# Kernel tuning notes

Hardware: AMD Instinct MI355X
Metric: run time of the kernel (lower is better)

## Reference

```python
import jax, jax.numpy as jnp
import numpy as np

B, T, D, H = 2, 2048, 1024, 16
HD = D // H  # 64
SCALE = 1.0 / np.sqrt(D).astype(np.float32)  # module uses 1/sqrt(mod_dim), not head_dim


def setup_inputs() -> dict:
    key = jax.random.key(0)
    k1, k2, k3 = jax.random.split(key, 3)
    x = jax.random.normal(k1, (B, T, D), dtype=jnp.float32)
    W_attn = jax.random.normal(k2, (3 * D, D), dtype=jnp.float32) * 0.02
    W_out = jax.random.normal(k3, (D, D), dtype=jnp.float32) * 0.02
    return {"x": x, "W_attn": W_attn, "W_out": W_out}


def reference(x, W_attn, W_out):
    b, t, d = x.shape
    # qkv projection (Linear, no bias): x @ W^T
    qkv = jnp.einsum('btd,ed->bte', x, W_attn)  # [b, t, 3d]
    q, k, v = jnp.split(qkv, 3, axis=-1)
    # [b, h, t, hd]
    q = q.reshape(b, t, H, HD).transpose(0, 2, 1, 3)
    k = k.reshape(b, t, H, HD).transpose(0, 2, 1, 3)
    v = v.reshape(b, t, H, HD).transpose(0, 2, 1, 3)
    # raw scores, causal mask applied before scaling (scale*-inf == -inf, so
    # equivalent to the original mask-then-scale order)
    att = jnp.einsum('bhqd,bhkd->bhqk', q, k)
    causal = jnp.tril(jnp.ones((t, t), dtype=bool))
    att = jnp.where(causal[None, None], att * SCALE, -jnp.inf)
    att = jax.nn.softmax(att, axis=-1)
    z = jnp.einsum('bhqk,bhkd->bhqd', att, v)
    z = z.transpose(0, 2, 1, 3).reshape(b, t, d)
    return jnp.einsum('btd,od->bto', z, W_out)
```

## Files before the change

kernel.cpp:

```cpp
#include <hip/hip_runtime.h>
#include <cstddef>

typedef unsigned short u16;
typedef __attribute__((ext_vector_type(4))) float floatx4;
typedef __attribute__((ext_vector_type(8))) short short8;

#define TT 2048
#define DD 1024
#define NH 16
#define ATT_SCALE (1.0f / 32.0f)
#define PSTR 72

__device__ __forceinline__ u16 f2bf(float f) {
  unsigned u = __builtin_bit_cast(unsigned, f);
  u += 0x7fffu + ((u >> 16) & 1u);
  return (u16)(u >> 16);
}

__device__ __forceinline__ unsigned pack2(float a, float b) {
#if __has_builtin(__builtin_amdgcn_cvt_pk_bf16_f32)
  auto t = __builtin_amdgcn_cvt_pk_bf16_f32(a, b);
  return __builtin_bit_cast(unsigned, t);
#else
  unsigned ua = __builtin_bit_cast(unsigned, a);
  ua += 0x7fffu + ((ua >> 16) & 1u);
  unsigned ub = __builtin_bit_cast(unsigned, b);
  ub += 0x7fffu + ((ub >> 16) & 1u);
  return (ua >> 16) | (ub & 0xffff0000u);
#endif
}

__device__ __forceinline__ void g2l16(const u16* g, u16* l) {
#if __has_builtin(__builtin_amdgcn_global_load_lds)
  __builtin_amdgcn_global_load_lds(
      (const __attribute__((address_space(1))) unsigned int*)g,
      (__attribute__((address_space(3))) unsigned int*)l, 16, 0, 0);
#else
  *(int4*)l = *(const int4*)g;
#endif
}

__device__ __forceinline__ short8 scale_q(short8 q) {
  short8 r;
#pragma unroll
  for (int i = 0; i < 8; ++i) {
    float f = __builtin_bit_cast(float, ((unsigned)(u16)q[i]) << 16) * ATT_SCALE;
    r[i] = (short)f2bf(f);
  }
  return r;
}

__global__ __launch_bounds__(256) void cvt3_kernel(const float* __restrict__ a,
                                                   const float* __restrict__ b,
                                                   const float* __restrict__ c,
                                                   u16* __restrict__ out,
                                                   int na, int nb, int nc) {
  int i = blockIdx.x * 256 + threadIdx.x;
  const float* src;
  int j;
  if (i < na) { src = a; j = i; }
  else if (i < na + nb) { src = b; j = i - na; }
  else if (i < na + nb + nc) { src = c; j = i - na - nb; }
  else return;
  float4 v = ((const float4*)src)[j];
  ((ushort4*)out)[i] = make_ushort4(f2bf(v.x), f2bf(v.y), f2bf(v.z), f2bf(v.w));
}

template <int MODE, int BN>
__global__ __launch_bounds__(256) void gemm_bt(const u16* __restrict__ A,
                                               const u16* __restrict__ Bm,
                                               void* __restrict__ C,
                                               u16* __restrict__ vt,
                                               int M, int N, int K) {
  constexpr int NT = BN / 32;
  __shared__ u16 As[128 * 32];
  __shared__ u16 Bs[BN * 32];
  const int tid = threadIdx.x;
  const int lane = tid & 63;
  const int wave = tid >> 6;
  const int quad = lane >> 4;
  const int l16 = lane & 15;
  const int wm = (wave >> 1) * 64;
  const int wn = (wave & 1) * (BN / 2);
  const int m0 = blockIdx.x * 128;
  const int n0 = blockIdx.y * BN;

  const int srow = wave * 16 + (lane >> 2);
  const int scol = (lane & 3) * 8;
  const int sl = wave * 512 + lane * 8;

  floatx4 acc[4][NT] = {};

  for (int k0 = 0; k0 < K; k0 += 32) {
    __syncthreads();
    g2l16(&A[(size_t)(m0 + srow) * K + k0 + scol], &As[sl]);
    g2l16(&A[(size_t)(m0 + 64 + srow) * K + k0 + scol], &As[2048 + sl]);
    g2l16(&Bm[(size_t)(n0 + srow) * K + k0 + scol], &Bs[sl]);
    if (BN == 128)
      g2l16(&Bm[(size_t)(n0 + 64 + srow) * K + k0 + scol], &Bs[2048 + sl]);
    __syncthreads();

    short8 af[4];
#pragma unroll
    for (int mt = 0; mt < 4; ++mt)
      af[mt] = *(const short8*)&As[(wm + mt * 16 + l16) * 32 + quad * 8];
#pragma unroll
    for (int nt = 0; nt < NT; ++nt) {
      short8 bf = *(const short8*)&Bs[(wn + nt * 16 + l16) * 32 + quad * 8];
#pragma unroll
      for (int mt = 0; mt < 4; ++mt)
        acc[mt][nt] = __builtin_amdgcn_mfma_f32_16x16x32_bf16(af[mt], bf, acc[mt][nt], 0, 0, 0);
    }
  }

  if (MODE == 2 && n0 >= 2048) {
    const int bidx = m0 >> 11;
    const int tbase = (m0 & 2047) + wm;
#pragma unroll
    for (int mt = 0; mt < 4; ++mt)
#pragma unroll
      for (int nt = 0; nt < NT; ++nt) {
        int gn = n0 + wn + nt * 16 + l16;
        size_t vrow = (size_t)(bidx * 1024 + gn - 2048);
        int t = tbase + mt * 16 + quad * 4;
        uint2 val;
        val.x = pack2(acc[mt][nt][0], acc[mt][nt][1]);
        val.y = pack2(acc[mt][nt][2], acc[mt][nt][3]);
        *(uint2*)&vt[vrow * TT + t] = val;
      }
  } else {
    const int cw = (MODE == 2) ? 2048 : N;
#pragma unroll
    for (int mt = 0; mt < 4; ++mt)
#pragma unroll
      for (int nt = 0; nt < NT; ++nt)
#pragma unroll
        for (int r = 0; r < 4; ++r) {
          int gm = m0 + wm + mt * 16 + quad * 4 + r;
          int gn = n0 + wn + nt * 16 + l16;
          float v = acc[mt][nt][r];
          if (MODE >= 1)
            ((u16*)C)[(size_t)gm * cw + gn] = f2bf(v);
          else
            ((float*)C)[(size_t)gm * cw + gn] = v;
        }
  }
}

__global__ __launch_bounds__(512) void attn_flash5(const u16* __restrict__ qk,
                                                   const u16* __restrict__ vt,
                                                   u16* __restrict__ z) {
  __shared__ u16 Ks[2][64 * PSTR];
  __shared__ u16 Vs[2][64 * PSTR];
  __shared__ u16 Ps[8][16 * PSTR];

  const int tid = threadIdx.x;
  const int lane = tid & 63;
  const int wave = tid >> 6;
  const int qs = wave & 3;
  const int par = wave >> 2;
  const int quad = lane >> 4;
  const int l16 = lane & 15;

  const int p = blockIdx.x;
  const int qtA = p, qtB = 31 - p;
  const int bh = blockIdx.y;
  const int b = bh >> 4, h = bh & 15;

  const size_t bbase = (size_t)b * TT * 2048;
  const u16* qg = qk + bbase + h * 64;
  const u16* kg = qk + bbase + 1024 + h * 64;
  const u16* vtg = vt + (size_t)bh * 64 * TT;

  short8 qfA[2], qfB[2];
  {
    const size_t ra = (size_t)(qtA * 64 + qs * 16 + l16) * 2048;
    const size_t rb = (size_t)(qtB * 64 + qs * 16 + l16) * 2048;
    qfA[0] = scale_q(*(const short8*)&qg[ra + quad * 8]);
    qfA[1] = scale_q(*(const short8*)&qg[ra + 32 + quad * 8]);
    qfB[0] = scale_q(*(const short8*)&qg[rb + quad * 8]);
    qfB[1] = scale_q(*(const short8*)&qg[rb + 32 + quad * 8]);
  }

  floatx4 OA[4] = {}, OB[4] = {};
  float psA[4] = {}, psB[4] = {};

  const int tsel = tid >> 8;
  const int t8 = tid & 255;
  const int str = t8 >> 2, sc = (t8 & 3) * 16;

  const int nktB = qtB + 1;
  const int M = (nktB + 1) >> 1;
  const int qrbA = qtA * 64 + qs * 16 + quad * 4;
  const int qrbB = qtB * 64 + qs * 16 + quad * 4;

  for (int m = 0; m < M; ++m) {
    const int kt = 2 * m + par;
    const int kt0 = kt * 64;
    __syncthreads();
    {
      const int kst = 2 * m + tsel;
      if (kst < nktB) {
        *(int4*)&Ks[tsel][str * PSTR + sc] =
            *(const int4*)&kg[(size_t)(kst * 64 + str) * 2048 + sc];
        *(int4*)&Ks[tsel][str * PSTR + sc + 8] =
            *(const int4*)&kg[(size_t)(kst * 64 + str) * 2048 + sc + 8];
        *(int4*)&Vs[tsel][str * PSTR + sc] =
            *(const int4*)&vtg[(size_t)str * TT + kst * 64 + sc];
        *(int4*)&Vs[tsel][str * PSTR + sc + 8] =
            *(const int4*)&vtg[(size_t)str * TT + kst * 64 + sc + 8];
      }
    }
    __syncthreads();

    if (kt < nktB) {
      floatx4 s[4];
#pragma unroll
      for (int nt = 0; nt < 4; ++nt) {
        short8 k0 = *(const short8*)&Ks[par][(nt * 16 + l16) * PSTR + quad * 8];
        short8 k1 = *(const short8*)&Ks[par][(nt * 16 + l16) * PSTR + 32 + quad * 8];
        floatx4 zz = {0.f, 0.f, 0.f, 0.f};
        s[nt] = __builtin_amdgcn_mfma_f32_16x16x32_bf16(qfB[0], k0, zz, 0, 0, 0);
        s[nt] = __builtin_amdgcn_mfma_f32_16x16x32_bf16(qfB[1], k1, s[nt], 0, 0, 0);
      }
      if (kt == qtB) {
#pragma unroll
        for (int nt = 0; nt < 4; ++nt)
#pragma unroll
          for (int r = 0; r < 4; ++r) {
            int kk = kt0 + nt * 16 + l16;
            float pv = (kk <= qrbB + r) ? __expf(s[nt][r]) : 0.f;
            psB[r] += pv;
            Ps[wave][(quad * 4 + r) * PSTR + nt * 16 + l16] = f2bf(pv);
          }
      } else {
#pragma unroll
        for (int nt = 0; nt < 4; ++nt)
#pragma unroll
          for (int r = 0; r < 4; ++r) {
            float pv = __expf(s[nt][r]);
            psB[r] += pv;
            Ps[wave][(quad * 4 + r) * PSTR + nt * 16 + l16] = f2bf(pv);
          }
      }
      {
        short8 p0 = *(const short8*)&Ps[wave][l16 * PSTR + quad * 8];
        short8 p1 = *(const short8*)&Ps[wave][l16 * PSTR + 32 + quad * 8];
#pragma unroll
        for (int nt = 0; nt < 4; ++nt) {
          short8 v0 = *(const short8*)&Vs[par][(nt * 16 + l16) * PSTR + quad * 8];
          short8 v1 = *(const short8*)&Vs[par][(nt * 16 + l16) * PSTR + 32 + quad * 8];
          OB[nt] = __builtin_amdgcn_mfma_f32_16x16x32_bf16(p0, v0, OB[nt], 0, 0, 0);
          OB[nt] = __builtin_amdgcn_mfma_f32_16x16x32_bf16(p1, v1, OB[nt], 0, 0, 0);
        }
      }

      if (kt <= qtA) {
#pragma unroll
        for (int nt = 0; nt < 4; ++nt) {
          short8 k0 = *(const short8*)&Ks[par][(nt * 16 + l16) * PSTR + quad * 8];
          short8 k1 = *(const short8*)&Ks[par][(nt * 16 + l16) * PSTR + 32 + quad * 8];
          floatx4 zz = {0.f, 0.f, 0.f, 0.f};
          s[nt] = __builtin_amdgcn_mfma_f32_16x16x32_bf16(qfA[0], k0, zz, 0, 0, 0);
          s[nt] = __builtin_amdgcn_mfma_f32_16x16x32_bf16(qfA[1], k1, s[nt], 0, 0, 0);
        }
        if (kt == qtA) {
#pragma unroll
          for (int nt = 0; nt < 4; ++nt)
#pragma unroll
            for (int r = 0; r < 4; ++r) {
              int kk = kt0 + nt * 16 + l16;
              float pv = (kk <= qrbA + r) ? __expf(s[nt][r]) : 0.f;
              psA[r] += pv;
              Ps[wave][(quad * 4 + r) * PSTR + nt * 16 + l16] = f2bf(pv);
            }
        } else {
#pragma unroll
          for (int nt = 0; nt < 4; ++nt)
#pragma unroll
            for (int r = 0; r < 4; ++r) {
              float pv = __expf(s[nt][r]);
              psA[r] += pv;
              Ps[wave][(quad * 4 + r) * PSTR + nt * 16 + l16] = f2bf(pv);
            }
        }
        short8 p0 = *(const short8*)&Ps[wave][l16 * PSTR + quad * 8];
        short8 p1 = *(const short8*)&Ps[wave][l16 * PSTR + 32 + quad * 8];
#pragma unroll
        for (int nt = 0; nt < 4; ++nt) {
          short8 v0 = *(const short8*)&Vs[par][(nt * 16 + l16) * PSTR + quad * 8];
          short8 v1 = *(const short8*)&Vs[par][(nt * 16 + l16) * PSTR + 32 + quad * 8];
          OA[nt] = __builtin_amdgcn_mfma_f32_16x16x32_bf16(p0, v0, OA[nt], 0, 0, 0);
          OA[nt] = __builtin_amdgcn_mfma_f32_16x16x32_bf16(p1, v1, OA[nt], 0, 0, 0);
        }
      }
    }
  }

#pragma unroll
  for (int off = 1; off < 16; off <<= 1)
#pragma unroll
    for (int r = 0; r < 4; ++r) {
      psA[r] += __shfl_xor(psA[r], off, 64);
      psB[r] += __shfl_xor(psB[r], off, 64);
    }

  float* red = (float*)Ps;
  float* lred = red + 4096;
  __syncthreads();
  if (par == 1) {
#pragma unroll
    for (int nt = 0; nt < 4; ++nt)
#pragma unroll
      for (int r = 0; r < 4; ++r)
        red[(qs * 16 + quad * 4 + r) * 64 + nt * 16 + l16] = OA[nt][r];
    if (l16 == 0)
#pragma unroll
      for (int r = 0; r < 4; ++r) lred[qs * 16 + quad * 4 + r] = psA[r];
  }
  __syncthreads();
  if (par == 0) {
#pragma unroll
    for (int r = 0; r < 4; ++r) {
      int row = qs * 16 + quad * 4 + r;
      float rl = 1.0f / (psA[r] + lred[row]);
      int qa = qtA * 64 + row;
#pragma unroll
      for (int nt = 0; nt < 4; ++nt) {
        float o = OA[nt][r] + red[row * 64 + nt * 16 + l16];
        z[(size_t)(b * TT + qa) * DD + h * 64 + nt * 16 + l16] = f2bf(o * rl);
      }
    }
  }
  __syncthreads();
  if (par == 1) {
#pragma unroll
    for (int nt = 0; nt < 4; ++nt)
#pragma unroll
      for (int r = 0; r < 4; ++r)
        red[(qs * 16 + quad * 4 + r) * 64 + nt * 16 + l16] = OB[nt][r];
    if (l16 == 0)
#pragma unroll
      for (int r = 0; r < 4; ++r) lred[qs * 16 + quad * 4 + r] = psB[r];
  }
  __syncthreads();
  if (par == 0) {
#pragma unroll
    for (int r = 0; r < 4; ++r) {
      int row = qs * 16 + quad * 4 + r;
      float rl = 1.0f / (psB[r] + lred[row]);
      int qb = qtB * 64 + row;
#pragma unroll
      for (int nt = 0; nt < 4; ++nt) {
        float o = OB[nt][r] + red[row * 64 + nt * 16 + l16];
        z[(size_t)(b * TT + qb) * DD + h * 64 + nt * 16 + l16] = f2bf(o * rl);
      }
    }
  }
}

extern "C" void kernel_launch(void* const* d_in, const int* in_sizes, int n_in,
                              void* d_out, int out_size, void* d_ws, size_t ws_size,
                              hipStream_t stream) {
  const float* x  = (const float*)d_in[0];
  const float* Wa = (const float*)d_in[1];
  const float* Wo = (const float*)d_in[2];
  float* out = (float*)d_out;

  u16* xb  = (u16*)d_ws;
  u16* Wab = xb  + (size_t)4096 * 1024;
  u16* Wob = Wab + (size_t)3072 * 1024;
  u16* qk  = Wob + (size_t)1024 * 1024;
  u16* z   = qk  + (size_t)4096 * 2048;
  u16* vt  = z   + (size_t)4096 * 1024;

  cvt3_kernel<<<8192, 256, 0, stream>>>(x, Wa, Wo, xb, 1048576, 786432, 262144);

  gemm_bt<2, 128><<<dim3(32, 24), 256, 0, stream>>>(xb, Wab, qk, vt, 4096, 3072, 1024);

  attn_flash5<<<dim3(16, 2 * NH), 512, 0, stream>>>(qk, vt, z);

  gemm_bt<0, 64><<<dim3(32, 16), 256, 0, stream>>>(z, Wob, out, nullptr, 4096, 1024, 1024);
}
```

Measured before the change: 179.3 us.

## Prefetch K/V into registers, interleave A/B tiles, use exp2 with folded log2e

The global loads for the next K/V tile are issued into registers before the current tile is computed, so load latency overlaps with MFMA work rather than sitting between barriers. K fragments are loaded from LDS once and shared by both query tiles. The two P tiles get separate LDS buffers so their PV MFMAs can interleave. log2(e) is folded into the Q scale so the kernel can use the hardware exp2, bf16 rounding of P uses a cheaper round-half-up, and launch bounds request 4 blocks per CU. The costs are more registers per thread and slightly different rounding of P.

Result: slower. 234.7 us (+30.9%).

```diff
diff --git a/kernel.cpp b/kernel.cpp
--- a/kernel.cpp
+++ b/kernel.cpp
@@ -8,13 +8,26 @@
 #define TT 2048
 #define DD 1024
 #define NH 16
-#define ATT_SCALE (1.0f / 32.0f)
+#define QSCALE (1.4426950408889634f / 32.0f)
 #define PSTR 72
 
 __device__ __forceinline__ u16 f2bf(float f) {
   unsigned u = __builtin_bit_cast(unsigned, f);
   u += 0x7fffu + ((u >> 16) & 1u);
   return (u16)(u >> 16);
+}
+
+__device__ __forceinline__ u16 f2bf_fast(float f) {
+  unsigned u = __builtin_bit_cast(unsigned, f);
+  return (u16)((u + 0x8000u) >> 16);
+}
+
+__device__ __forceinline__ float fexp2(float x) {
+#if __has_builtin(__builtin_amdgcn_exp2f)
+  return __builtin_amdgcn_exp2f(x);
+#else
+  return exp2f(x);
+#endif
 }
 
 __device__ __forceinline__ unsigned pack2(float a, float b) {
@@ -44,7 +57,7 @@
   short8 r;
 #pragma unroll
   for (int i = 0; i < 8; ++i) {
-    float f = __builtin_bit_cast(float, ((unsigned)(u16)q[i]) << 16) * ATT_SCALE;
+    float f = __builtin_bit_cast(float, ((unsigned)(u16)q[i]) << 16) * QSCALE;
     r[i] = (short)f2bf(f);
   }
   return r;
@@ -147,12 +160,12 @@
   }
 }
 
-__global__ __launch_bounds__(512) void attn_flash5(const u16* __restrict__ qk,
-                                                   const u16* __restrict__ vt,
-                                                   u16* __restrict__ z) {
+__global__ __launch_bounds__(512, 4) void attn_flash6(const u16* __restrict__ qk,
+                                                      const u16* __restrict__ vt,
+                                                      u16* __restrict__ z) {
   __shared__ u16 Ks[2][64 * PSTR];
   __shared__ u16 Vs[2][64 * PSTR];
-  __shared__ u16 Ps[8][16 * PSTR];
+  __shared__ u16 Ps[8][2][16 * PSTR];
 
   const int tid = threadIdx.x;
   const int lane = tid & 63;
@@ -194,104 +207,120 @@
   const int qrbA = qtA * 64 + qs * 16 + quad * 4;
   const int qrbB = qtB * 64 + qs * 16 + quad * 4;
 
+  int4 kr0 = *(const int4*)&kg[(size_t)(tsel * 64 + str) * 2048 + sc];
+  int4 kr1 = *(const int4*)&kg[(size_t)(tsel * 64 + str) * 2048 + sc + 8];
+  int4 vr0 = *(const int4*)&vtg[(size_t)str * TT + tsel * 64 + sc];
+  int4 vr1 = *(const int4*)&vtg[(size_t)str * TT + tsel * 64 + sc + 8];
+  bool have = true;
+
   for (int m = 0; m < M; ++m) {
+    __syncthreads();
+    if (have) {
+      *(int4*)&Ks[tsel][str * PSTR + sc] = kr0;
+      *(int4*)&Ks[tsel][str * PSTR + sc + 8] = kr1;
+      *(int4*)&Vs[tsel][str * PSTR + sc] = vr0;
+      *(int4*)&Vs[tsel][str * PSTR + sc + 8] = vr1;
+    }
+    __syncthreads();
+
+    {
+      const int kst = 2 * (m + 1) + tsel;
+      have = kst < nktB;
+      if (have) {
+        kr0 = *(const int4*)&kg[(size_t)(kst * 64 + str) * 2048 + sc];
+        kr1 = *(const int4*)&kg[(size_t)(kst * 64 + str) * 2048 + sc + 8];
+        vr0 = *(const int4*)&vtg[(size_t)str * TT + kst * 64 + sc];
+        vr1 = *(const int4*)&vtg[(size_t)str * TT + kst * 64 + sc + 8];
+      }
+    }
+
     const int kt = 2 * m + par;
-    const int kt0 = kt * 64;
-    __syncthreads();
-    {
-      const int kst = 2 * m + tsel;
-      if (kst < nktB) {
-        *(int4*)&Ks[tsel][str * PSTR + sc] =
-            *(const int4*)&kg[(size_t)(kst * 64 + str) * 2048 + sc];
-        *(int4*)&Ks[tsel][str * PSTR + sc + 8] =
-            *(const int4*)&kg[(size_t)(kst * 64 + str) * 2048 + sc + 8];
-        *(int4*)&Vs[tsel][str * PSTR + sc] =
-            *(const int4*)&vtg[(size_t)str * TT + kst * 64 + sc];
-        *(int4*)&Vs[tsel][str * PSTR + sc + 8] =
-            *(const int4*)&vtg[(size_t)str * TT + kst * 64 + sc + 8];
-      }
-    }
-    __syncthreads();
-
     if (kt < nktB) {
-      floatx4 s[4];
+      const int kt0 = kt * 64;
+      const bool actA = (kt <= qtA);
+
+      short8 kf0[4], kf1[4];
 #pragma unroll
       for (int nt = 0; nt < 4; ++nt) {
-        short8 k0 = *(const short8*)&Ks[par][(nt * 16 + l16) * PSTR + quad * 8];
-        short8 k1 = *(const short8*)&Ks[par][(nt * 16 + l16) * PSTR + 32 + quad * 8];
+        kf0[nt] = *(const short8*)&Ks[par][(nt * 16 + l16) * PSTR + quad * 8];
+        kf1[nt] = *(const short8*)&Ks[par][(nt * 16 + l16) * PSTR + 32 + quad * 8];
+      }
+
+      floatx4 sB[4], sA[4];
+#pragma unroll
+      for (int nt = 0; nt < 4; ++nt) {
         floatx4 zz = {0.f, 0.f, 0.f, 0.f};
-        s[nt] = __builtin_amdgcn_mfma_f32_16x16x32_bf16(qfB[0], k0, zz, 0, 0, 0);
-        s[nt] = __builtin_amdgcn_mfma_f32_16x16x32_bf16(qfB[1], k1, s[nt], 0, 0, 0);
-      }
+        sB[nt] = __builtin_amdgcn_mfma_f32_16x16x32_bf16(qfB[0], kf0[nt], zz, 0, 0, 0);
+        sB[nt] = __builtin_amdgcn_mfma_f32_16x16x32_bf16(qfB[1], kf1[nt], sB[nt], 0, 0, 0);
+      }
+      if (actA) {
+#pragma unroll
+        for (int nt = 0; nt < 4; ++nt) {
+          floatx4 zz = {0.f, 0.f, 0.f, 0.f};
+          sA[nt] = __builtin_amdgcn_mfma_f32_16x16x32_bf16(qfA[0], kf0[nt], zz, 0, 0, 0);
+          sA[nt] = __builtin_amdgcn_mfma_f32_16x16x32_bf16(qfA[1], kf1[nt], sA[nt], 0, 0, 0);
+        }
+      }
+
       if (kt == qtB) {
 #pragma unroll
         for (int nt = 0; nt < 4; ++nt)
 #pragma unroll
           for (int r = 0; r < 4; ++r) {
             int kk = kt0 + nt * 16 + l16;
-            float pv = (kk <= qrbB + r) ? __expf(s[nt][r]) : 0.f;
+            float pv = (kk <= qrbB + r) ? fexp2(sB[nt][r]) : 0.f;
             psB[r] += pv;
-            Ps[wave][(quad * 4 + r) * PSTR + nt * 16 + l16] = f2bf(pv);
+            Ps[wave][1][(quad * 4 + r) * PSTR + nt * 16 + l16] = f2bf_fast(pv);
           }
       } else {
 #pragma unroll
         for (int nt = 0; nt < 4; ++nt)
 #pragma unroll
           for (int r = 0; r < 4; ++r) {
-            float pv = __expf(s[nt][r]);
+            float pv = fexp2(sB[nt][r]);
             psB[r] += pv;
-            Ps[wave][(quad * 4 + r) * PSTR + nt * 16 + l16] = f2bf(pv);
+            Ps[wave][1][(quad * 4 + r) * PSTR + nt * 16 + l16] = f2bf_fast(pv);
           }
       }
-      {
-        short8 p0 = *(const short8*)&Ps[wave][l16 * PSTR + quad * 8];
-        short8 p1 = *(const short8*)&Ps[wave][l16 * PSTR + 32 + quad * 8];
-#pragma unroll
-        for (int nt = 0; nt < 4; ++nt) {
-          short8 v0 = *(const short8*)&Vs[par][(nt * 16 + l16) * PSTR + quad * 8];
-          short8 v1 = *(const short8*)&Vs[par][(nt * 16 + l16) * PSTR + 32 + quad * 8];
-          OB[nt] = __builtin_amdgcn_mfma_f32_16x16x32_bf16(p0, v0, OB[nt], 0, 0, 0);
-          OB[nt] = __builtin_amdgcn_mfma_f32_16x16x32_bf16(p1, v1, OB[nt], 0, 0, 0);
-        }
-      }
-
-      if (kt <= qtA) {
-#pragma unroll
-        for (int nt = 0; nt < 4; ++nt) {
-          short8 k0 = *(const short8*)&Ks[par][(nt * 16 + l16) * PSTR + quad * 8];
-          short8 k1 = *(const short8*)&Ks[par][(nt * 16 + l16) * PSTR + 32 + quad * 8];
-          floatx4 zz = {0.f, 0.f, 0.f, 0.f};
-          s[nt] = __builtin_amdgcn_mfma_f32_16x16x32_bf16(qfA[0], k0, zz, 0, 0, 0);
-          s[nt] = __builtin_amdgcn_mfma_f32_16x16x32_bf16(qfA[1], k1, s[nt], 0, 0, 0);
-        }
+      if (actA) {
         if (kt == qtA) {
 #pragma unroll
           for (int nt = 0; nt < 4; ++nt)
 #pragma unroll
             for (int r = 0; r < 4; ++r) {
               int kk = kt0 + nt * 16 + l16;
-              float pv = (kk <= qrbA + r) ? __expf(s[nt][r]) : 0.f;
+              float pv = (kk <= qrbA + r) ? fexp2(sA[nt][r]) : 0.f;
               psA[r] += pv;
-              Ps[wave][(quad * 4 + r) * PSTR + nt * 16 + l16] = f2bf(pv);
+              Ps[wave][0][(quad * 4 + r) * PSTR + nt * 16 + l16] = f2bf_fast(pv);
             }
         } else {
 #pragma unroll
           for (int nt = 0; nt < 4; ++nt)
 #pragma unroll
             for (int r = 0; r < 4; ++r) {
-              float pv = __expf(s[nt][r]);
+              float pv = fexp2(sA[nt][r]);
               psA[r] += pv;
-              Ps[wave][(quad * 4 + r) * PSTR + nt * 16 + l16] = f2bf(pv);
+              Ps[wave][0][(quad * 4 + r) * PSTR + nt * 16 + l16] = f2bf_fast(pv);
             }
         }
-        short8 p0 = *(const short8*)&Ps[wave][l16 * PSTR + quad * 8];
-        short8 p1 = *(const short8*)&Ps[wave][l16 * PSTR + 32 + quad * 8];
-#pragma unroll
-        for (int nt = 0; nt < 4; ++nt) {
-          short8 v0 = *(const short8*)&Vs[par][(nt * 16 + l16) * PSTR + quad * 8];
-          short8 v1 = *(const short8*)&Vs[par][(nt * 16 + l16) * PSTR + 32 + quad * 8];
-          OA[nt] = __builtin_amdgcn_mfma_f32_16x16x32_bf16(p0, v0, OA[nt], 0, 0, 0);
-          OA[nt] = __builtin_amdgcn_mfma_f32_16x16x32_bf16(p1, v1, OA[nt], 0, 0, 0);
+      }
+
+      short8 pB0 = *(const short8*)&Ps[wave][1][l16 * PSTR + quad * 8];
+      short8 pB1 = *(const short8*)&Ps[wave][1][l16 * PSTR + 32 + quad * 8];
+      short8 pA0, pA1;
+      if (actA) {
+        pA0 = *(const short8*)&Ps[wave][0][l16 * PSTR + quad * 8];
+        pA1 = *(const short8*)&Ps[wave][0][l16 * PSTR + 32 + quad * 8];
+      }
+#pragma unroll
+      for (int nt = 0; nt < 4; ++nt) {
+        short8 v0 = *(const short8*)&Vs[par][(nt * 16 + l16) * PSTR + quad * 8];
+        short8 v1 = *(const short8*)&Vs[par][(nt * 16 + l16) * PSTR + 32 + quad * 8];
+        OB[nt] = __builtin_amdgcn_mfma_f32_16x16x32_bf16(pB0, v0, OB[nt], 0, 0, 0);
+        OB[nt] = __builtin_amdgcn_mfma_f32_16x16x32_bf16(pB1, v1, OB[nt], 0, 0, 0);
+        if (actA) {
+          OA[nt] = __builtin_amdgcn_mfma_f32_16x16x32_bf16(pA0, v0, OA[nt], 0, 0, 0);
+          OA[nt] = __builtin_amdgcn_mfma_f32_16x16x32_bf16(pA1, v1, OA[nt], 0, 0, 0);
         }
       }
     }
@@ -378,7 +407,7 @@
 
   gemm_bt<2, 128><<<dim3(32, 24), 256, 0, stream>>>(xb, Wab, qk, vt, 4096, 3072, 1024);
 
-  attn_flash5<<<dim3(16, 2 * NH), 512, 0, stream>>>(qk, vt, z);
+  attn_flash6<<<dim3(16, 2 * NH), 512, 0, stream>>>(qk, vt, z);
 
   gemm_bt<0, 64><<<dim3(32, 16), 256, 0, stream>>>(z, Wob, out, nullptr, 4096, 1024, 1024);
 }
```
